# Optimization experiments

Hardware: AMD Instinct MI355X
Metric: run time of the kernel (lower is better)

## Reference

```python
import jax, jax.numpy as jnp
import numpy as np

EPS = 1e-7  # K.epsilon()
B, S, W1, W2, D = 256, 4, 64, 128, 300
HID = 4


def setup_inputs() -> dict:
    key = jax.random.key(0)
    k1, k2, k3, k4, k5, k6, k7 = jax.random.split(key, 7)
    return {
        "tuple1": jax.random.normal(k1, (B, S, W1, D), dtype=jnp.float32),
        "tuple2": jax.random.normal(k2, (B, S, W2, D), dtype=jnp.float32),
        "mask1": jax.random.randint(k3, (B, S, W1), 0, 2, dtype=jnp.int32),
        "mask2": jax.random.randint(k4, (B, S, W2), 0, 2, dtype=jnp.int32),
        "threshold": jax.random.normal(k5, (), dtype=jnp.float32),
        "W_hidden": jax.random.normal(k6, (S, HID), dtype=jnp.float32) * 0.5,
        "W_score": jax.random.normal(k7, (HID, 1), dtype=jnp.float32) * 0.5,
    }


def reference(tuple1, tuple2, mask1, mask2, threshold, W_hidden, W_score):
    # Pairwise dot-product similarity between every tuple1 word and tuple2 word per slot.
    sim = jnp.einsum("bswd,bsvd->bswv", tuple1, tuple2)  # (B, S, W1, W2)
    m1 = mask1.astype(jnp.float32)
    m2 = mask2.astype(jnp.float32)
    overlap = (sim >= threshold).astype(jnp.float32)
    overlap = overlap * m1[:, :, :, None] * m2[:, :, None, :]
    slot_overlap = jnp.sum(overlap, axis=(2, 3))  # (B, S)
    count1 = jnp.sum(m1, axis=2)  # (B, S)
    divisor = jnp.where(count1 == 0, EPS, count1)
    normalized = slot_overlap / divisor  # (B, S)
    h = jnp.tanh(normalized @ W_hidden)  # (B, HID)
    return jax.nn.sigmoid(h @ W_score)  # (B, 1)
```

## Files before the change

### kernel.cpp

```cpp
#include <hip/hip_runtime.h>
#include <math.h>

#define B_   256
#define S_   4
#define W1_  64
#define W2_  128
#define D_   300
#define HID_ 4
#define KT   60
#define NKT  5
#define PADK 64

__global__ __launch_bounds__(256) void sim_count_kernel(
    const float* __restrict__ t1, const float* __restrict__ t2,
    const int* __restrict__ m1, const int* __restrict__ m2,
    const float* __restrict__ thr_p, float* __restrict__ norm_out)
{
    __shared__ float As[W1_ * PADK];
    __shared__ float Bs[W2_ * PADK];
    __shared__ int widx[W1_];
    __shared__ int vidx[W2_];
    __shared__ int cntA, cntB, cntOv;

    const int bs  = blockIdx.x;
    const int tid = threadIdx.x;
    const float thr = *thr_p;

    if (tid == 0) { cntA = 0; cntB = 0; cntOv = 0; }
    __syncthreads();

    if (tid < W1_) {
        if (m1[bs * W1_ + tid] != 0) {
            int p = atomicAdd(&cntA, 1);
            widx[p] = tid;
        }
    } else if (tid < W1_ + W2_) {
        int v = tid - W1_;
        if (m2[bs * W2_ + v] != 0) {
            int p = atomicAdd(&cntB, 1);
            vidx[p] = v;
        }
    }
    __syncthreads();

    const int nA = cntA, nB = cntB;
    const int Ra = (nA + 3) >> 2;
    const int Cb = (nB + 7) >> 3;
    const int Ta = Ra * Cb;

    int tr = 0, tc = 0;
    const bool active = (tid < Ta);
    if (active) { tr = tid / Cb; tc = tid - tr * Cb; }
    const int swa = tr & 7;
    const int swb = tc & 7;

    float acc[4][8];
    #pragma unroll
    for (int i = 0; i < 4; ++i)
        #pragma unroll
        for (int j = 0; j < 8; ++j) acc[i][j] = 0.f;

    const float* t1b = t1 + (size_t)bs * W1_ * D_;
    const float* t2b = t2 + (size_t)bs * W2_ * D_;

    for (int kt = 0; kt < NKT; ++kt) {
        const int k0 = kt * KT;
        for (int idx = tid; idx < nA * (KT / 4); idx += 256) {
            int a = idx / (KT / 4);
            int f = idx - a * (KT / 4);
            const float4 val = *reinterpret_cast<const float4*>(
                t1b + (size_t)widx[a] * D_ + k0 + 4 * f);
            *reinterpret_cast<float4*>(
                &As[a * PADK + 4 * (f ^ ((a >> 2) & 7))]) = val;
        }
        for (int idx = tid; idx < nB * (KT / 4); idx += 256) {
            int v = idx / (KT / 4);
            int f = idx - v * (KT / 4);
            const float4 val = *reinterpret_cast<const float4*>(
                t2b + (size_t)vidx[v] * D_ + k0 + 4 * f);
            *reinterpret_cast<float4*>(
                &Bs[v * PADK + 4 * (f ^ ((v >> 3) & 7))]) = val;
        }
        __syncthreads();

        if (active) {
            #pragma unroll
            for (int g = 0; g < KT / 4; ++g) {
                float4 av[4];
                float4 bv[8];
                #pragma unroll
                for (int i = 0; i < 4; ++i)
                    av[i] = *reinterpret_cast<const float4*>(
                        &As[(4 * tr + i) * PADK + 4 * (g ^ swa)]);
                #pragma unroll
                for (int j = 0; j < 8; ++j)
                    bv[j] = *reinterpret_cast<const float4*>(
                        &Bs[(8 * tc + j) * PADK + 4 * (g ^ swb)]);
                #pragma unroll
                for (int i = 0; i < 4; ++i)
                    #pragma unroll
                    for (int j = 0; j < 8; ++j) {
                        acc[i][j] = fmaf(av[i].x, bv[j].x, acc[i][j]);
                        acc[i][j] = fmaf(av[i].y, bv[j].y, acc[i][j]);
                        acc[i][j] = fmaf(av[i].z, bv[j].z, acc[i][j]);
                        acc[i][j] = fmaf(av[i].w, bv[j].w, acc[i][j]);
                    }
            }
        }
        __syncthreads();
    }

    int lc = 0;
    if (active) {
        const int ilim = min(nA - 4 * tr, 4);
        const int jlim = min(nB - 8 * tc, 8);
        #pragma unroll
        for (int i = 0; i < 4; ++i)
            #pragma unroll
            for (int j = 0; j < 8; ++j)
                lc += ((i < ilim) & (j < jlim) & (acc[i][j] >= thr)) ? 1 : 0;
    }
    #pragma unroll
    for (int o = 32; o > 0; o >>= 1) lc += __shfl_down(lc, o);
    if ((tid & 63) == 0 && lc != 0) atomicAdd(&cntOv, lc);
    __syncthreads();

    if (tid == 0) {
        float divisor = (nA == 0) ? 1e-7f : (float)nA;
        norm_out[bs] = (float)cntOv / divisor;
    }
}

__global__ __launch_bounds__(256) void head_kernel(
    const float* __restrict__ norm,
    const float* __restrict__ Wh,
    const float* __restrict__ Ws,
    float* __restrict__ out)
{
    int b = blockIdx.x * blockDim.x + threadIdx.x;
    if (b >= B_) return;
    float4 n = *reinterpret_cast<const float4*>(norm + b * 4);
    float score = 0.f;
    #pragma unroll
    for (int j = 0; j < HID_; ++j) {
        float h = n.x * Wh[0 * HID_ + j] + n.y * Wh[1 * HID_ + j]
                + n.z * Wh[2 * HID_ + j] + n.w * Wh[3 * HID_ + j];
        h = tanhf(h);
        score += h * Ws[j];
    }
    out[b] = 1.f / (1.f + expf(-score));
}

extern "C" void kernel_launch(void* const* d_in, const int* in_sizes, int n_in,
                              void* d_out, int out_size, void* d_ws, size_t ws_size,
                              hipStream_t stream)
{
    const float* t1  = (const float*)d_in[0];
    const float* t2  = (const float*)d_in[1];
    const int*   m1  = (const int*)d_in[2];
    const int*   m2  = (const int*)d_in[3];
    const float* thr = (const float*)d_in[4];
    const float* Wh  = (const float*)d_in[5];
    const float* Ws  = (const float*)d_in[6];
    float* out  = (float*)d_out;
    float* norm = (float*)d_ws;

    sim_count_kernel<<<B_ * S_, 256, 0, stream>>>(t1, t2, m1, m2, thr, norm);
    head_kernel<<<1, 256, 0, stream>>>(norm, Wh, Ws, out);
}
```

Before: 313.0 us.

## Replace FP32 shared-memory GEMM with split-bf16 MFMA register-direct kernel

The FP32 FMA tile loop that staged inputs through shared memory is replaced by MFMA 16x16x32 bf16 instructions. Each input is split into hi/lo bf16 parts and three MFMAs per product approximate FP32 accuracy. Operands load straight from global memory into registers with double-buffered prefetch, and masks are applied after accumulation instead of compacting rows. Per-slot counts go to global atomics after a memset, and nA is recomputed in the head kernel. The cost is three MFMAs per tile, an extra memset launch, and possible threshold flips from the residual precision loss.

```diff
diff --git a/kernel.cpp b/kernel.cpp
--- a/kernel.cpp
+++ b/kernel.cpp
@@ -7,144 +7,177 @@
 #define W2_  128
 #define D_   300
 #define HID_ 4
-#define KT   60
-#define NKT  5
-#define PADK 64
-
-__global__ __launch_bounds__(256) void sim_count_kernel(
+
+typedef float          fx4   __attribute__((ext_vector_type(4)));
+typedef short          s16x8 __attribute__((ext_vector_type(8)));
+typedef unsigned int   ux4   __attribute__((ext_vector_type(4)));
+
+__device__ __forceinline__ unsigned bf16_rne(float x) {
+    unsigned u = __float_as_uint(x);
+    return (u + 0x7FFFu + ((u >> 16) & 1u)) >> 16;
+}
+
+__device__ __forceinline__ void cvt8(const fx4 x0, const fx4 x1, s16x8& hi, s16x8& lo) {
+    ux4 hu, lu;
+#pragma unroll
+    for (int p = 0; p < 4; ++p) {
+        float a = (p < 2) ? x0[2 * p]     : x1[2 * p - 4];
+        float b = (p < 2) ? x0[2 * p + 1] : x1[2 * p - 3];
+        unsigned ha = bf16_rne(a), hb = bf16_rne(b);
+        float haf = __uint_as_float(ha << 16);
+        float hbf = __uint_as_float(hb << 16);
+        unsigned la = bf16_rne(a - haf), lb = bf16_rne(b - hbf);
+        hu[p] = ha | (hb << 16);
+        lu[p] = la | (lb << 16);
+    }
+    hi = __builtin_bit_cast(s16x8, hu);
+    lo = __builtin_bit_cast(s16x8, lu);
+}
+
+__global__ __launch_bounds__(256, 2) void sim_count_mfma(
     const float* __restrict__ t1, const float* __restrict__ t2,
     const int* __restrict__ m1, const int* __restrict__ m2,
-    const float* __restrict__ thr_p, float* __restrict__ norm_out)
+    const float* __restrict__ thr_p, int* __restrict__ cnt)
 {
-    __shared__ float As[W1_ * PADK];
-    __shared__ float Bs[W2_ * PADK];
-    __shared__ int widx[W1_];
-    __shared__ int vidx[W2_];
-    __shared__ int cntA, cntB, cntOv;
-
-    const int bs  = blockIdx.x;
-    const int tid = threadIdx.x;
+    const int slot = blockIdx.x;
+    const int tid  = threadIdx.x;
+    const int l    = tid & 63;
+    const int w    = tid >> 6;
+    const int rowHalf = w >> 1, colHalf = w & 1;
+    const int lr   = l & 15;
+    const int lg8  = (l >> 4) * 8;
     const float thr = *thr_p;
 
-    if (tid == 0) { cntA = 0; cntB = 0; cntOv = 0; }
-    __syncthreads();
-
-    if (tid < W1_) {
-        if (m1[bs * W1_ + tid] != 0) {
-            int p = atomicAdd(&cntA, 1);
-            widx[p] = tid;
-        }
-    } else if (tid < W1_ + W2_) {
-        int v = tid - W1_;
-        if (m2[bs * W2_ + v] != 0) {
-            int p = atomicAdd(&cntB, 1);
-            vidx[p] = v;
-        }
-    }
-    __syncthreads();
-
-    const int nA = cntA, nB = cntB;
-    const int Ra = (nA + 3) >> 2;
-    const int Cb = (nB + 7) >> 3;
-    const int Ta = Ra * Cb;
-
-    int tr = 0, tc = 0;
-    const bool active = (tid < Ta);
-    if (active) { tr = tid / Cb; tc = tid - tr * Cb; }
-    const int swa = tr & 7;
-    const int swb = tc & 7;
-
-    float acc[4][8];
-    #pragma unroll
-    for (int i = 0; i < 4; ++i)
-        #pragma unroll
-        for (int j = 0; j < 8; ++j) acc[i][j] = 0.f;
-
-    const float* t1b = t1 + (size_t)bs * W1_ * D_;
-    const float* t2b = t2 + (size_t)bs * W2_ * D_;
-
-    for (int kt = 0; kt < NKT; ++kt) {
-        const int k0 = kt * KT;
-        for (int idx = tid; idx < nA * (KT / 4); idx += 256) {
-            int a = idx / (KT / 4);
-            int f = idx - a * (KT / 4);
-            const float4 val = *reinterpret_cast<const float4*>(
-                t1b + (size_t)widx[a] * D_ + k0 + 4 * f);
-            *reinterpret_cast<float4*>(
-                &As[a * PADK + 4 * (f ^ ((a >> 2) & 7))]) = val;
-        }
-        for (int idx = tid; idx < nB * (KT / 4); idx += 256) {
-            int v = idx / (KT / 4);
-            int f = idx - v * (KT / 4);
-            const float4 val = *reinterpret_cast<const float4*>(
-                t2b + (size_t)vidx[v] * D_ + k0 + 4 * f);
-            *reinterpret_cast<float4*>(
-                &Bs[v * PADK + 4 * (f ^ ((v >> 3) & 7))]) = val;
-        }
-        __syncthreads();
-
-        if (active) {
-            #pragma unroll
-            for (int g = 0; g < KT / 4; ++g) {
-                float4 av[4];
-                float4 bv[8];
-                #pragma unroll
-                for (int i = 0; i < 4; ++i)
-                    av[i] = *reinterpret_cast<const float4*>(
-                        &As[(4 * tr + i) * PADK + 4 * (g ^ swa)]);
-                #pragma unroll
-                for (int j = 0; j < 8; ++j)
-                    bv[j] = *reinterpret_cast<const float4*>(
-                        &Bs[(8 * tc + j) * PADK + 4 * (g ^ swb)]);
-                #pragma unroll
-                for (int i = 0; i < 4; ++i)
-                    #pragma unroll
-                    for (int j = 0; j < 8; ++j) {
-                        acc[i][j] = fmaf(av[i].x, bv[j].x, acc[i][j]);
-                        acc[i][j] = fmaf(av[i].y, bv[j].y, acc[i][j]);
-                        acc[i][j] = fmaf(av[i].z, bv[j].z, acc[i][j]);
-                        acc[i][j] = fmaf(av[i].w, bv[j].w, acc[i][j]);
-                    }
+    const float* aP[2];
+    const float* bP[4];
+#pragma unroll
+    for (int rt = 0; rt < 2; ++rt)
+        aP[rt] = t1 + (size_t)slot * W1_ * D_ + (size_t)(rowHalf * 32 + rt * 16 + lr) * D_ + lg8;
+#pragma unroll
+    for (int ct = 0; ct < 4; ++ct)
+        bP[ct] = t2 + (size_t)slot * W2_ * D_ + (size_t)(colHalf * 64 + ct * 16 + lr) * D_ + lg8;
+
+    fx4 acc[2][4];
+#pragma unroll
+    for (int rt = 0; rt < 2; ++rt)
+#pragma unroll
+        for (int ct = 0; ct < 4; ++ct) {
+            fx4 z; z[0] = 0.f; z[1] = 0.f; z[2] = 0.f; z[3] = 0.f;
+            acc[rt][ct] = z;
+        }
+
+    auto issue_full = [&](fx4 (&SA)[2][2], fx4 (&SB)[4][2], int t) {
+#pragma unroll
+        for (int rt = 0; rt < 2; ++rt) {
+            const float* p = aP[rt] + t * 32;
+            SA[rt][0] = *(const fx4*)p;
+            SA[rt][1] = *(const fx4*)(p + 4);
+        }
+#pragma unroll
+        for (int ct = 0; ct < 4; ++ct) {
+            const float* p = bP[ct] + t * 32;
+            SB[ct][0] = *(const fx4*)p;
+            SB[ct][1] = *(const fx4*)(p + 4);
+        }
+    };
+    auto issue_tail = [&](fx4 (&SA)[2][2], fx4 (&SB)[4][2]) {
+        fx4 z; z[0] = 0.f; z[1] = 0.f; z[2] = 0.f; z[3] = 0.f;
+#pragma unroll
+        for (int rt = 0; rt < 2; ++rt) {
+            const float* p = aP[rt] + 288;
+            SA[rt][0] = z; SA[rt][1] = z;
+            if (lg8 < 16) SA[rt][0] = *(const fx4*)p;
+            if (lg8 == 0) SA[rt][1] = *(const fx4*)(p + 4);
+        }
+#pragma unroll
+        for (int ct = 0; ct < 4; ++ct) {
+            const float* p = bP[ct] + 288;
+            SB[ct][0] = z; SB[ct][1] = z;
+            if (lg8 < 16) SB[ct][0] = *(const fx4*)p;
+            if (lg8 == 0) SB[ct][1] = *(const fx4*)(p + 4);
+        }
+    };
+    auto compute = [&](fx4 (&SA)[2][2], fx4 (&SB)[4][2]) {
+        s16x8 ah[2], al[2];
+#pragma unroll
+        for (int rt = 0; rt < 2; ++rt) cvt8(SA[rt][0], SA[rt][1], ah[rt], al[rt]);
+#pragma unroll
+        for (int ct = 0; ct < 4; ++ct) {
+            s16x8 bh, bl;
+            cvt8(SB[ct][0], SB[ct][1], bh, bl);
+#pragma unroll
+            for (int rt = 0; rt < 2; ++rt) {
+                acc[rt][ct] = __builtin_amdgcn_mfma_f32_16x16x32_bf16(ah[rt], bh, acc[rt][ct], 0, 0, 0);
+                acc[rt][ct] = __builtin_amdgcn_mfma_f32_16x16x32_bf16(ah[rt], bl, acc[rt][ct], 0, 0, 0);
+                acc[rt][ct] = __builtin_amdgcn_mfma_f32_16x16x32_bf16(al[rt], bh, acc[rt][ct], 0, 0, 0);
             }
         }
-        __syncthreads();
-    }
+    };
+
+    fx4 s0A[2][2], s0B[4][2], s1A[2][2], s1B[4][2];
+    issue_full(s0A, s0B, 0);
+#pragma unroll
+    for (int tt = 0; tt < 4; ++tt) {
+        issue_full(s1A, s1B, 2 * tt + 1);
+        compute(s0A, s0B);
+        issue_full(s0A, s0B, 2 * tt + 2);
+        compute(s1A, s1B);
+    }
+    issue_tail(s1A, s1B);
+    compute(s0A, s0B);
+    compute(s1A, s1B);
+
+    int am[2][4];
+#pragma unroll
+    for (int rt = 0; rt < 2; ++rt)
+#pragma unroll
+        for (int r = 0; r < 4; ++r)
+            am[rt][r] = m1[slot * W1_ + rowHalf * 32 + rt * 16 + (l >> 4) * 4 + r];
+    int bm[4];
+#pragma unroll
+    for (int ct = 0; ct < 4; ++ct)
+        bm[ct] = m2[slot * W2_ + colHalf * 64 + ct * 16 + lr];
 
     int lc = 0;
-    if (active) {
-        const int ilim = min(nA - 4 * tr, 4);
-        const int jlim = min(nB - 8 * tc, 8);
-        #pragma unroll
-        for (int i = 0; i < 4; ++i)
-            #pragma unroll
-            for (int j = 0; j < 8; ++j)
-                lc += ((i < ilim) & (j < jlim) & (acc[i][j] >= thr)) ? 1 : 0;
-    }
-    #pragma unroll
+#pragma unroll
+    for (int rt = 0; rt < 2; ++rt)
+#pragma unroll
+        for (int ct = 0; ct < 4; ++ct)
+#pragma unroll
+            for (int r = 0; r < 4; ++r)
+                lc += ((acc[rt][ct][r] >= thr) & (am[rt][r] != 0) & (bm[ct] != 0)) ? 1 : 0;
+#pragma unroll
     for (int o = 32; o > 0; o >>= 1) lc += __shfl_down(lc, o);
-    if ((tid & 63) == 0 && lc != 0) atomicAdd(&cntOv, lc);
-    __syncthreads();
-
-    if (tid == 0) {
-        float divisor = (nA == 0) ? 1e-7f : (float)nA;
-        norm_out[bs] = (float)cntOv / divisor;
-    }
-}
-
-__global__ __launch_bounds__(256) void head_kernel(
-    const float* __restrict__ norm,
+    if (l == 0) atomicAdd(&cnt[slot], lc);
+}
+
+__global__ __launch_bounds__(256) void finalize_head(
+    const int* __restrict__ cnt, const int* __restrict__ m1,
     const float* __restrict__ Wh,
     const float* __restrict__ Ws,
     float* __restrict__ out)
 {
     int b = blockIdx.x * blockDim.x + threadIdx.x;
     if (b >= B_) return;
-    float4 n = *reinterpret_cast<const float4*>(norm + b * 4);
+    float n[4];
+#pragma unroll
+    for (int s = 0; s < 4; ++s) {
+        const int slot = b * 4 + s;
+        int nA = 0;
+        const int4* mp = (const int4*)(m1 + slot * W1_);
+#pragma unroll
+        for (int g = 0; g < 16; ++g) {
+            int4 v = mp[g];
+            nA += (v.x != 0) + (v.y != 0) + (v.z != 0) + (v.w != 0);
+        }
+        const float divisor = (nA == 0) ? 1e-7f : (float)nA;
+        n[s] = (float)cnt[slot] / divisor;
+    }
     float score = 0.f;
-    #pragma unroll
+#pragma unroll
     for (int j = 0; j < HID_; ++j) {
-        float h = n.x * Wh[0 * HID_ + j] + n.y * Wh[1 * HID_ + j]
-                + n.z * Wh[2 * HID_ + j] + n.w * Wh[3 * HID_ + j];
+        float h = n[0] * Wh[0 * HID_ + j] + n[1] * Wh[1 * HID_ + j]
+                + n[2] * Wh[2 * HID_ + j] + n[3] * Wh[3 * HID_ + j];
         h = tanhf(h);
         score += h * Ws[j];
     }
@@ -162,9 +195,10 @@
     const float* thr = (const float*)d_in[4];
     const float* Wh  = (const float*)d_in[5];
     const float* Ws  = (const float*)d_in[6];
-    float* out  = (float*)d_out;
-    float* norm = (float*)d_ws;
-
-    sim_count_kernel<<<B_ * S_, 256, 0, stream>>>(t1, t2, m1, m2, thr, norm);
-    head_kernel<<<1, 256, 0, stream>>>(norm, Wh, Ws, out);
-}
+    float* out = (float*)d_out;
+    int*   cnt = (int*)d_ws;
+
+    hipMemsetAsync(cnt, 0, B_ * S_ * sizeof(int), stream);
+    sim_count_mfma<<<B_ * S_, 256, 0, stream>>>(t1, t2, m1, m2, thr, cnt);
+    finalize_head<<<1, 256, 0, stream>>>(cnt, m1, Wh, Ws, out);
+}
```

New measurement: 340.8 us. 1.09x slower.
